# Kernel tuning notes

Hardware: AMD Instinct MI355X
Metric: run time of the kernel (lower is better)

Reference implementation:

```python
import jax, jax.numpy as jnp
import numpy as np

H, DK, DV = 16, 128, 128
EPS = 1e-6


def _causal_dw_conv(x, w):
    # depthwise causal conv, no bias. x: [B,T,C], w: [K,C]
    K = w.shape[0]
    T = x.shape[1]
    xp = jnp.pad(x, ((0, 0), (K - 1, 0), (0, 0)))
    out = w[0] * xp[:, 0:T, :]
    for i in range(1, K):
        out = out + w[i] * xp[:, i:i + T, :]
    return out


def _rmsnorm(h, w):
    hf = h.astype(jnp.float32)
    var = jnp.mean(hf * hf, axis=-1, keepdims=True)
    return (hf * jax.lax.rsqrt(var + EPS)).astype(h.dtype) * w


def _l2norm(x):
    return x * jax.lax.rsqrt(jnp.sum(x * x, axis=-1, keepdims=True) + EPS)


def setup_inputs() -> dict:
    key = jax.random.key(0)
    ks = jax.random.split(key, 32)
    B, T, D = 1, 1024, 2048
    LOW, I = 128, 8192
    KD, VD = H * DK, H * DV
    s = 0.02
    f = jnp.float32
    return {
        "x": jax.random.normal(ks[0], (B, T, D), f),
        "wq": jax.random.normal(ks[1], (D, KD), f) * s,
        "wk": jax.random.normal(ks[2], (D, KD), f) * s,
        "wv": jax.random.normal(ks[3], (D, VD), f) * s,
        "conv_q": jax.random.normal(ks[4], (4, KD), f) * 0.2,
        "conv_k": jax.random.normal(ks[5], (4, KD), f) * 0.2,
        "conv_v": jax.random.normal(ks[6], (4, VD), f) * 0.2,
        "wfa": jax.random.normal(ks[7], (D, LOW), f) * s,
        "wfb": jax.random.normal(ks[8], (LOW, H), f) * s,
        "wb": jax.random.normal(ks[9], (D, H), f) * s,
        "wga": jax.random.normal(ks[10], (D, LOW), f) * s,
        "wgb": jax.random.normal(ks[11], (LOW, VD), f) * s,
        "a_log": jax.random.normal(ks[12], (H,), f) * 0.1,
        "dt_bias": jnp.ones((H,), f),
        "o_norm_w": jnp.ones((DV,), f),
        "wo": jax.random.normal(ks[13], (VD, D), f) * s,
        "ln1_w": jnp.ones((D,), f),
        "ln2_w": jnp.ones((D,), f),
        "w_gate": jax.random.normal(ks[14], (D, I), f) * s,
        "w_up": jax.random.normal(ks[15], (D, I), f) * s,
        "w_down": jax.random.normal(ks[16], (I, D), f) * s,
    }


def reference(x, wq, wk, wv, conv_q, conv_k, conv_v, wfa, wfb, wb, wga, wgb,
              a_log, dt_bias, o_norm_w, wo, ln1_w, ln2_w, w_gate, w_up, w_down):
    B, T, D = x.shape
    # ---- pre-attention RMSNorm ----
    h = _rmsnorm(x, ln1_w)
    # ---- KDA: projections + causal depthwise conv + silu ----
    q = jax.nn.silu(_causal_dw_conv(h @ wq, conv_q)).reshape(B, T, H, DK)
    k = jax.nn.silu(_causal_dw_conv(h @ wk, conv_k)).reshape(B, T, H, DK)
    v = jax.nn.silu(_causal_dw_conv(h @ wv, conv_v)).reshape(B, T, H, DV)
    q = _l2norm(q) * (DK ** -0.5)
    k = _l2norm(k)
    # decay gate (per head, log-space, negative) and beta update gate
    g = -jnp.exp(a_log) * jax.nn.softplus((h @ wfa) @ wfb + dt_bias)  # [B,T,H]
    beta = jax.nn.sigmoid(h @ wb)                                      # [B,T,H]

    # ---- gated delta-rule linear attention (recurrent scan over time) ----
    def step(S, inp):
        qt, kt, vt, gt, bt = inp                 # [B,H,Dk],[B,H,Dk],[B,H,Dv],[B,H],[B,H]
        S = S * jnp.exp(gt)[..., None, None]     # decay state [B,H,Dk,Dv]
        kS = jnp.einsum('bhk,bhkv->bhv', kt, S)  # current prediction for k_t
        S = S + bt[..., None, None] * (kt[..., :, None] * (vt - kS)[..., None, :])
        ot = jnp.einsum('bhk,bhkv->bhv', qt, S)
        return S, ot

    S0 = jnp.zeros((B, H, DK, DV), x.dtype)
    xs = (q.transpose(1, 0, 2, 3), k.transpose(1, 0, 2, 3), v.transpose(1, 0, 2, 3),
          g.transpose(1, 0, 2), beta.transpose(1, 0, 2))
    _, o = jax.lax.scan(step, S0, xs)
    o = o.transpose(1, 0, 2, 3)                  # [B,T,H,Dv]

    # ---- gated RMSNorm on output + output projection ----
    gate = ((h @ wga) @ wgb).reshape(B, T, H, DV)
    o = _rmsnorm(o, o_norm_w) * jax.nn.silu(gate.astype(jnp.float32))
    o = o.astype(x.dtype).reshape(B, T, H * DV) @ wo
    x = x + o
    # ---- MLP block (SwiGLU) ----
    h2 = _rmsnorm(x, ln2_w)
    mlp = (jax.nn.silu(h2 @ w_gate) * (h2 @ w_up)) @ w_down
    return x + mlp
```

## Files before the change

### kernel.cpp

```cpp
#include <hip/hip_runtime.h>
#include <hip/hip_bf16.h>

typedef __attribute__((ext_vector_type(8))) short short8;
typedef __attribute__((ext_vector_type(4))) float f32x4;
typedef __attribute__((ext_vector_type(8))) unsigned short u16x8;
typedef __attribute__((ext_vector_type(4))) unsigned short u16x4;

__device__ __forceinline__ unsigned short f2bf(float f) {
  unsigned u = __float_as_uint(f);
  u += 0x7fffu + ((u >> 16) & 1u);
  return (unsigned short)(u >> 16);
}
__device__ __forceinline__ float silu_f(float x) { return x / (1.f + __expf(-x)); }
__device__ __forceinline__ float red16(float v) {
  v += __shfl_xor(v, 1); v += __shfl_xor(v, 2);
  v += __shfl_xor(v, 4); v += __shfl_xor(v, 8);
  return v;
}
template <int CTRL>
__device__ __forceinline__ float dpp_mv(float v) {
  return __int_as_float(__builtin_amdgcn_update_dpp(0, __float_as_int(v), CTRL, 0xF, 0xF, true));
}
__device__ __forceinline__ float red16d(float v) {
  v += dpp_mv<0xB1>(v);
  v += dpp_mv<0x4E>(v);
  v += dpp_mv<0x141>(v);
  v += dpp_mv<0x140>(v);
  return v;
}
__device__ __forceinline__ void gload16(const void* g, void* l) {
  __builtin_amdgcn_global_load_lds((const __attribute__((address_space(1))) void*)g,
                                   (__attribute__((address_space(3))) void*)l, 16, 0, 0);
}

struct TDesc { const float* src; unsigned short* dst; int R, C, tilesX, start; };
struct TDescs { TDesc d[11]; };

__global__ void __launch_bounds__(256) trans_all_kernel(TDescs ds) {
  __shared__ float tile[64][65];
  const int bid = blockIdx.x;
  int e = 0;
#pragma unroll
  for (int i = 1; i < 11; i++) e = (bid >= ds.d[i].start) ? i : e;
  const float* __restrict__ src = ds.d[e].src;
  unsigned short* __restrict__ dst = ds.d[e].dst;
  const int R = ds.d[e].R, C = ds.d[e].C;
  const int local = bid - ds.d[e].start;
  const int c0 = (local % ds.d[e].tilesX) * 64;
  const int r0 = (local / ds.d[e].tilesX) * 64;
  const int tid = threadIdx.x;
  const int l = tid & 15, g = tid >> 4;
#pragma unroll
  for (int i = 0; i < 4; i++) {
    const int r = r0 + g + 16 * i;
    const int c = c0 + 4 * l;
    if (r < R) {
      if (c + 3 < C) {
        float4 v = *(const float4*)(src + (size_t)r * C + c);
        tile[4 * l + 0][g + 16 * i] = v.x;
        tile[4 * l + 1][g + 16 * i] = v.y;
        tile[4 * l + 2][g + 16 * i] = v.z;
        tile[4 * l + 3][g + 16 * i] = v.w;
      } else {
#pragma unroll
        for (int j = 0; j < 4; j++)
          if (c + j < C) tile[4 * l + j][g + 16 * i] = src[(size_t)r * C + c + j];
      }
    }
  }
  __syncthreads();
#pragma unroll
  for (int i = 0; i < 4; i++) {
    const int cc = c0 + g + 16 * i;
    const int rc = r0 + 4 * l;
    if (cc < C) {
      if (rc + 3 < R) {
        u16x4 o;
        o[0] = f2bf(tile[g + 16 * i][4 * l + 0]);
        o[1] = f2bf(tile[g + 16 * i][4 * l + 1]);
        o[2] = f2bf(tile[g + 16 * i][4 * l + 2]);
        o[3] = f2bf(tile[g + 16 * i][4 * l + 3]);
        *(u16x4*)(dst + (size_t)cc * R + rc) = o;
      } else {
#pragma unroll
        for (int j = 0; j < 4; j++)
          if (rc + j < R) dst[(size_t)cc * R + rc + j] = f2bf(tile[g + 16 * i][4 * l + j]);
      }
    }
  }
}

__global__ void __launch_bounds__(256) rmsnorm_bf16_kernel(const float* __restrict__ x,
                                                           const float* __restrict__ w,
                                                           unsigned short* __restrict__ outb) {
  const int t = blockIdx.x, tid = threadIdx.x;
  const float* xr = x + (size_t)t * 2048 + tid * 8;
  float4 v0 = *(const float4*)xr, v1 = *(const float4*)(xr + 4);
  float ss = v0.x*v0.x + v0.y*v0.y + v0.z*v0.z + v0.w*v0.w
           + v1.x*v1.x + v1.y*v1.y + v1.z*v1.z + v1.w*v1.w;
#pragma unroll
  for (int m = 1; m < 64; m <<= 1) ss += __shfl_xor(ss, m);
  __shared__ float sb[4];
  if ((tid & 63) == 0) sb[tid >> 6] = ss;
  __syncthreads();
  float rn = rsqrtf((sb[0] + sb[1] + sb[2] + sb[3]) * (1.f / 2048.f) + 1e-6f);
  const float* wr = w + tid * 8;
  float4 w0 = *(const float4*)wr, w1 = *(const float4*)(wr + 4);
  u16x8 r;
  r[0]=f2bf(v0.x*rn*w0.x); r[1]=f2bf(v0.y*rn*w0.y); r[2]=f2bf(v0.z*rn*w0.z); r[3]=f2bf(v0.w*rn*w0.w);
  r[4]=f2bf(v1.x*rn*w1.x); r[5]=f2bf(v1.y*rn*w1.y); r[6]=f2bf(v1.z*rn*w1.z); r[7]=f2bf(v1.w*rn*w1.w);
  *(u16x8*)(outb + (size_t)t * 2048 + tid * 8) = r;
}

__global__ void __launch_bounds__(256) add5_rmsnorm_kernel(const float* __restrict__ x,
                                                           const float* __restrict__ y1,
                                                           const float* __restrict__ y2,
                                                           const float* __restrict__ y3,
                                                           const float* __restrict__ y4,
                                                           const float* __restrict__ w,
                                                           float* __restrict__ x1,
                                                           unsigned short* __restrict__ h2b) {
  const int t = blockIdx.x, tid = threadIdx.x;
  const int c = tid * 8;
  const size_t off = (size_t)t * 2048 + c;
  float s[8]; float ss = 0.f;
  float4 a0 = *(const float4*)(x + off),  a1 = *(const float4*)(x + off + 4);
  float4 b0 = *(const float4*)(y1 + off), b1 = *(const float4*)(y1 + off + 4);
  float4 c0 = *(const float4*)(y2 + off), c1 = *(const float4*)(y2 + off + 4);
  float4 d0 = *(const float4*)(y3 + off), d1 = *(const float4*)(y3 + off + 4);
  float4 e0 = *(const float4*)(y4 + off), e1 = *(const float4*)(y4 + off + 4);
  s[0]=a0.x+b0.x+c0.x+d0.x+e0.x; s[1]=a0.y+b0.y+c0.y+d0.y+e0.y;
  s[2]=a0.z+b0.z+c0.z+d0.z+e0.z; s[3]=a0.w+b0.w+c0.w+d0.w+e0.w;
  s[4]=a1.x+b1.x+c1.x+d1.x+e1.x; s[5]=a1.y+b1.y+c1.y+d1.y+e1.y;
  s[6]=a1.z+b1.z+c1.z+d1.z+e1.z; s[7]=a1.w+b1.w+c1.w+d1.w+e1.w;
#pragma unroll
  for (int j = 0; j < 8; j++) ss += s[j] * s[j];
#pragma unroll
  for (int m = 1; m < 64; m <<= 1) ss += __shfl_xor(ss, m);
  __shared__ float sb[4];
  if ((tid & 63) == 0) sb[tid >> 6] = ss;
  __syncthreads();
  float rn = rsqrtf((sb[0] + sb[1] + sb[2] + sb[3]) * (1.f / 2048.f) + 1e-6f);
  float* xo = x1 + off;
  *(float4*)xo = *(float4*)&s[0];
  *(float4*)(xo + 4) = *(float4*)&s[4];
  const float* wr = w + c;
  float4 w0 = *(const float4*)wr, w1 = *(const float4*)(wr + 4);
  float wv[8] = {w0.x,w0.y,w0.z,w0.w,w1.x,w1.y,w1.z,w1.w};
  u16x8 r;
#pragma unroll
  for (int j = 0; j < 8; j++) r[j] = f2bf(s[j] * rn * wv[j]);
  *(u16x8*)(h2b + off) = r;
}

__global__ void __launch_bounds__(256) gemm_bt_kernel(const unsigned short* __restrict__ A,
                                                      const unsigned short* __restrict__ Bt,
                                                      float* __restrict__ C,
                                                      int M, int N, int K, int lda, int ldb) {
  __shared__ unsigned short As[128][32];
  __shared__ unsigned short Bs[128][32];
  const int tid = threadIdx.x;
  const int m0 = blockIdx.x << 7, n0 = blockIdx.y << 7;
  const int wave = tid >> 6, lane = tid & 63;
  const int wm = (wave >> 1) << 6, wn = (wave & 1) << 6;
  const int lrow = lane >> 2, lcol = lane & 3;
  const int ar0 = wave * 16 + lrow;
  const int ar1 = ar0 + 64;
  int br0 = n0 + ar0; br0 = br0 < N ? br0 : N - 1;
  int br1 = n0 + ar1; br1 = br1 < N ? br1 : N - 1;
  const unsigned short* Aptr0 = A + (size_t)(m0 + ar0) * lda + ((lcol ^ (ar0 & 3)) << 3);
  const unsigned short* Aptr1 = A + (size_t)(m0 + ar1) * lda + ((lcol ^ (ar1 & 3)) << 3);
  const unsigned short* Bptr0 = Bt + (size_t)br0 * ldb + ((lcol ^ (ar0 & 3)) << 3);
  const unsigned short* Bptr1 = Bt + (size_t)br1 * ldb + ((lcol ^ (ar1 & 3)) << 3);
  unsigned short* lA0 = &As[wave * 16][0];
  unsigned short* lA1 = &As[64 + wave * 16][0];
  unsigned short* lB0 = &Bs[wave * 16][0];
  unsigned short* lB1 = &Bs[64 + wave * 16][0];
  const int frow = lane & 15, fkb = lane >> 4;
  f32x4 acc[4][4];
#pragma unroll
  for (int i = 0; i < 4; i++)
#pragma unroll
    for (int j = 0; j < 4; j++) acc[i][j] = (f32x4){0.f, 0.f, 0.f, 0.f};

  for (int k0 = 0; k0 < K; k0 += 32) {
    gload16(Aptr0 + k0, lA0);
    gload16(Aptr1 + k0, lA1);
    gload16(Bptr0 + k0, lB0);
    gload16(Bptr1 + k0, lB1);
    __syncthreads();
    short8 af[4], bfr[4];
#pragma unroll
    for (int i = 0; i < 4; i++) {
      int ra = wm + i * 16 + frow;
      af[i] = *(const short8*)&As[ra][(fkb ^ (ra & 3)) << 3];
      int rb = wn + i * 16 + frow;
      bfr[i] = *(const short8*)&Bs[rb][(fkb ^ (rb & 3)) << 3];
    }
#pragma unroll
    for (int i = 0; i < 4; i++)
#pragma unroll
      for (int j = 0; j < 4; j++)
        acc[i][j] = __builtin_amdgcn_mfma_f32_16x16x32_bf16(af[i], bfr[j], acc[i][j], 0, 0, 0);
    __syncthreads();
  }
  const int crow = (lane >> 4) << 2, ccol = lane & 15;
#pragma unroll
  for (int i = 0; i < 4; i++) {
    const int gr = m0 + wm + i * 16 + crow;
#pragma unroll
    for (int j = 0; j < 4; j++) {
      const int gc = n0 + wn + j * 16 + ccol;
      if (gc < N) {
#pragma unroll
        for (int r = 0; r < 4; r++) C[(size_t)(gr + r) * N + gc] = acc[i][j][r];
      }
    }
  }
}

__global__ void __launch_bounds__(256) gemm_bt_splitk4_kernel(const unsigned short* __restrict__ Abase,
                                                              const unsigned short* __restrict__ Btbase,
                                                              float* __restrict__ C0,
                                                              float* __restrict__ C1,
                                                              float* __restrict__ C2,
                                                              float* __restrict__ C3,
                                                              int M, int N, int Kq,
                                                              int lda, int ldb) {
  const unsigned short* A = Abase + (size_t)blockIdx.z * Kq;
  const unsigned short* Bt = Btbase + (size_t)blockIdx.z * Kq;
  float* C = (blockIdx.z == 0) ? C0 : (blockIdx.z == 1) ? C1 : (blockIdx.z == 2) ? C2 : C3;
  __shared__ unsigned short As[128][32];
  __shared__ unsigned short Bs[128][32];
  const int tid = threadIdx.x;
  const int m0 = blockIdx.x << 7, n0 = blockIdx.y << 7;
  const int wave = tid >> 6, lane = tid & 63;
  const int wm = (wave >> 1) << 6, wn = (wave & 1) << 6;
  const int lrow = lane >> 2, lcol = lane & 3;
  const int ar0 = wave * 16 + lrow;
  const int ar1 = ar0 + 64;
  int br0 = n0 + ar0; br0 = br0 < N ? br0 : N - 1;
  int br1 = n0 + ar1; br1 = br1 < N ? br1 : N - 1;
  const unsigned short* Aptr0 = A + (size_t)(m0 + ar0) * lda + ((lcol ^ (ar0 & 3)) << 3);
  const unsigned short* Aptr1 = A + (size_t)(m0 + ar1) * lda + ((lcol ^ (ar1 & 3)) << 3);
  const unsigned short* Bptr0 = Bt + (size_t)br0 * ldb + ((lcol ^ (ar0 & 3)) << 3);
  const unsigned short* Bptr1 = Bt + (size_t)br1 * ldb + ((lcol ^ (ar1 & 3)) << 3);
  unsigned short* lA0 = &As[wave * 16][0];
  unsigned short* lA1 = &As[64 + wave * 16][0];
  unsigned short* lB0 = &Bs[wave * 16][0];
  unsigned short* lB1 = &Bs[64 + wave * 16][0];
  const int frow = lane & 15, fkb = lane >> 4;
  f32x4 acc[4][4];
#pragma unroll
  for (int i = 0; i < 4; i++)
#pragma unroll
    for (int j = 0; j < 4; j++) acc[i][j] = (f32x4){0.f, 0.f, 0.f, 0.f};

  for (int k0 = 0; k0 < Kq; k0 += 32) {
    gload16(Aptr0 + k0, lA0);
    gload16(Aptr1 + k0, lA1);
    gload16(Bptr0 + k0, lB0);
    gload16(Bptr1 + k0, lB1);
    __syncthreads();
    short8 af[4], bfr[4];
#pragma unroll
    for (int i = 0; i < 4; i++) {
      int ra = wm + i * 16 + frow;
      af[i] = *(const short8*)&As[ra][(fkb ^ (ra & 3)) << 3];
      int rb = wn + i * 16 + frow;
      bfr[i] = *(const short8*)&Bs[rb][(fkb ^ (rb & 3)) << 3];
    }
#pragma unroll
    for (int i = 0; i < 4; i++)
#pragma unroll
      for (int j = 0; j < 4; j++)
        acc[i][j] = __builtin_amdgcn_mfma_f32_16x16x32_bf16(af[i], bfr[j], acc[i][j], 0, 0, 0);
    __syncthreads();
  }
  const int crow = (lane >> 4) << 2, ccol = lane & 15;
#pragma unroll
  for (int i = 0; i < 4; i++) {
    const int gr = m0 + wm + i * 16 + crow;
#pragma unroll
    for (int j = 0; j < 4; j++) {
      const int gc = n0 + wn + j * 16 + ccol;
      if (gc < N) {
#pragma unroll
        for (int r = 0; r < 4; r++) C[(size_t)(gr + r) * N + gc] = acc[i][j][r];
      }
    }
  }
}

__global__ void __launch_bounds__(256) gemm_dual_swiglu_kernel(const unsigned short* __restrict__ A,
                                                               const unsigned short* __restrict__ Bt,
                                                               unsigned short* __restrict__ mid) {
  __shared__ unsigned short As[128][32];
  __shared__ unsigned short B1s[128][32];
  __shared__ unsigned short B2s[128][32];
  const int tid = threadIdx.x;
  const int m0 = blockIdx.x << 7, n0 = blockIdx.y << 7;
  const int wave = tid >> 6, lane = tid & 63;
  const int wm = (wave >> 1) << 6, wn = (wave & 1) << 6;
  const int lrow = lane >> 2, lcol = lane & 3;
  const int ar0 = wave * 16 + lrow;
  const int ar1 = ar0 + 64;
  const unsigned short* Aptr0 = A + (size_t)(m0 + ar0) * 2048 + ((lcol ^ (ar0 & 3)) << 3);
  const unsigned short* Aptr1 = A + (size_t)(m0 + ar1) * 2048 + ((lcol ^ (ar1 & 3)) << 3);
  const unsigned short* B1p0 = Bt + (size_t)(n0 + ar0) * 2048 + ((lcol ^ (ar0 & 3)) << 3);
  const unsigned short* B1p1 = Bt + (size_t)(n0 + ar1) * 2048 + ((lcol ^ (ar1 & 3)) << 3);
  const unsigned short* B2p0 = B1p0 + (size_t)8192 * 2048;
  const unsigned short* B2p1 = B1p1 + (size_t)8192 * 2048;
  unsigned short* lA0 = &As[wave * 16][0];
  unsigned short* lA1 = &As[64 + wave * 16][0];
  unsigned short* lB10 = &B1s[wave * 16][0];
  unsigned short* lB11 = &B1s[64 + wave * 16][0];
  unsigned short* lB20 = &B2s[wave * 16][0];
  unsigned short* lB21 = &B2s[64 + wave * 16][0];
  const int frow = lane & 15, fkb = lane >> 4;
  f32x4 acc1[4][4], acc2[4][4];
#pragma unroll
  for (int i = 0; i < 4; i++)
#pragma unroll
    for (int j = 0; j < 4; j++) {
      acc1[i][j] = (f32x4){0.f, 0.f, 0.f, 0.f};
      acc2[i][j] = (f32x4){0.f, 0.f, 0.f, 0.f};
    }
  for (int k0 = 0; k0 < 2048; k0 += 32) {
    gload16(Aptr0 + k0, lA0);
    gload16(Aptr1 + k0, lA1);
    gload16(B1p0 + k0, lB10);
    gload16(B1p1 + k0, lB11);
    gload16(B2p0 + k0, lB20);
    gload16(B2p1 + k0, lB21);
    __syncthreads();
    short8 af[4], b1f[4], b2f[4];
#pragma unroll
    for (int i = 0; i < 4; i++) {
      int ra = wm + i * 16 + frow;
      af[i] = *(const short8*)&As[ra][(fkb ^ (ra & 3)) << 3];
      int rb = wn + i * 16 + frow;
      b1f[i] = *(const short8*)&B1s[rb][(fkb ^ (rb & 3)) << 3];
      b2f[i] = *(const short8*)&B2s[rb][(fkb ^ (rb & 3)) << 3];
    }
#pragma unroll
    for (int i = 0; i < 4; i++)
#pragma unroll
      for (int j = 0; j < 4; j++) {
        acc1[i][j] = __builtin_amdgcn_mfma_f32_16x16x32_bf16(af[i], b1f[j], acc1[i][j], 0, 0, 0);
        acc2[i][j] = __builtin_amdgcn_mfma_f32_16x16x32_bf16(af[i], b2f[j], acc2[i][j], 0, 0, 0);
      }
    __syncthreads();
  }
  const int crow = (lane >> 4) << 2, ccol = lane & 15;
#pragma unroll
  for (int i = 0; i < 4; i++) {
    const int gr = m0 + wm + i * 16 + crow;
#pragma unroll
    for (int j = 0; j < 4; j++) {
      const int gc = n0 + wn + j * 16 + ccol;
#pragma unroll
      for (int r = 0; r < 4; r++)
        mid[(size_t)(gr + r) * 8192 + gc] = f2bf(silu_f(acc1[i][j][r]) * acc2[i][j][r]);
    }
  }
}

__global__ void __launch_bounds__(256) conv_gates_kernel(const float* __restrict__ proj,
                                                         const float* __restrict__ cq,
                                                         const float* __restrict__ ck,
                                                         const float* __restrict__ cv,
                                                         const float* __restrict__ small,
                                                         const float* __restrict__ wfb,
                                                         const float* __restrict__ a_log,
                                                         const float* __restrict__ dtb,
                                                         float* __restrict__ q, float* __restrict__ k,
                                                         float* __restrict__ v,
                                                         float4* __restrict__ g4,
                                                         unsigned short* __restrict__ gab) {
  __shared__ float qksh[16];
  const int t = blockIdx.x, tid = threadIdx.x;
  const int c = tid << 3;
  float aq[8] = {0,0,0,0,0,0,0,0}, ak[8] = {0,0,0,0,0,0,0,0}, av[8] = {0,0,0,0,0,0,0,0};
#pragma unroll
  for (int i = 0; i < 4; i++) {
    const int tt = t + i - 3;
    if (tt < 0) continue;
    const float* pr = proj + (size_t)tt * 6144;
    float pq[8], pk[8], pv[8], w0[8], w1[8], w2[8];
    *(float4*)&pq[0] = *(const float4*)(pr + c);        *(float4*)&pq[4] = *(const float4*)(pr + c + 4);
    *(float4*)&pk[0] = *(const float4*)(pr + 2048 + c); *(float4*)&pk[4] = *(const float4*)(pr + 2048 + c + 4);
    *(float4*)&pv[0] = *(const float4*)(pr + 4096 + c); *(float4*)&pv[4] = *(const float4*)(pr + 4096 + c + 4);
    *(float4*)&w0[0] = *(const float4*)(cq + i * 2048 + c); *(float4*)&w0[4] = *(const float4*)(cq + i * 2048 + c + 4);
    *(float4*)&w1[0] = *(const float4*)(ck + i * 2048 + c); *(float4*)&w1[4] = *(const float4*)(ck + i * 2048 + c + 4);
    *(float4*)&w2[0] = *(const float4*)(cv + i * 2048 + c); *(float4*)&w2[4] = *(const float4*)(cv + i * 2048 + c + 4);
#pragma unroll
    for (int j = 0; j < 8; j++) { aq[j] += w0[j]*pq[j]; ak[j] += w1[j]*pk[j]; av[j] += w2[j]*pv[j]; }
  }
  float sq[8], sk[8], sv[8]; float ssq = 0.f, ssk = 0.f;
#pragma unroll
  for (int j = 0; j < 8; j++) {
    sq[j] = silu_f(aq[j]); ssq += sq[j]*sq[j];
    sk[j] = silu_f(ak[j]); ssk += sk[j]*sk[j];
    sv[j] = silu_f(av[j]);
  }
  ssq = red16(ssq); ssk = red16(ssk);
  const float rq = rsqrtf(ssq + 1e-6f) * 0.08838834764831845f;
  const float rk = rsqrtf(ssk + 1e-6f);
  float oq[8], ok[8]; float qkl = 0.f;
#pragma unroll
  for (int j = 0; j < 8; j++) { oq[j] = sq[j]*rq; ok[j] = sk[j]*rk; qkl += oq[j]*ok[j]; }
  qkl = red16(qkl);
  if ((tid & 15) == 0) qksh[tid >> 4] = qkl;
  float* qo = q + (size_t)t * 2048 + c;
  *(float4*)qo = *(float4*)&oq[0]; *(float4*)(qo + 4) = *(float4*)&oq[4];
  float* ko = k + (size_t)t * 2048 + c;
  *(float4*)ko = *(float4*)&ok[0]; *(float4*)(ko + 4) = *(float4*)&ok[4];
  float* vo = v + (size_t)t * 2048 + c;
  *(float4*)vo = *(float4*)&sv[0]; *(float4*)(vo + 4) = *(float4*)&sv[4];
  __syncthreads();
  if (tid < 128) {
    const float* srow = small + (size_t)t * 272;
    const int hh = tid >> 3, j = tid & 7;
    float d = 0.f;
#pragma unroll
    for (int i = 0; i < 16; i++) d += srow[j * 16 + i] * wfb[(j * 16 + i) * 16 + hh];
    d += __shfl_xor(d, 1); d += __shfl_xor(d, 2); d += __shfl_xor(d, 4);
    if (j == 0) {
      d += dtb[hh];
      float sp = (d > 20.f) ? d : log1pf(expf(d));
      float eg = expf(-expf(a_log[hh]) * sp);
      float bt = 1.f / (1.f + expf(-srow[128 + hh]));
      g4[t * 16 + hh] = make_float4(eg, bt, qksh[hh], 0.f);
    }
    gab[(size_t)t * 128 + tid] = f2bf(srow[144 + tid]);
  }
}

struct Slot { float4 k0, k1, q0, q1; float eg, qk, btv, bteg; };

__device__ __forceinline__ void load_slot(Slot& X, const float* kb, const float* qb,
                                          const float* vb, const float4* g4b, int tt) {
  const float* kp = kb + (size_t)tt * 2048;
  const float* qp = qb + (size_t)tt * 2048;
  X.k0 = *(const float4*)kp; X.k1 = *(const float4*)(kp + 4);
  X.q0 = *(const float4*)qp; X.q1 = *(const float4*)(qp + 4);
  float4 g = g4b[(size_t)tt * 16];
  float v = vb[(size_t)tt * 2048];
  X.eg = g.x; X.qk = g.z;
  X.btv = g.y * v;
  X.bteg = g.y * g.x;
}

__device__ __forceinline__ void step_slot(const Slot& X, float (&S)[8], float* ob,
                                          bool dostore, int tt) {
  float a0 = fmaf(X.k1.x, S[4], X.k0.x * S[0]);
  float a1 = fmaf(X.k1.y, S[5], X.k0.y * S[1]);
  float a2 = fmaf(X.k1.z, S[6], X.k0.z * S[2]);
  float a3 = fmaf(X.k1.w, S[7], X.k0.w * S[3]);
  float b0 = fmaf(X.q1.x, S[4], X.q0.x * S[0]);
  float b1 = fmaf(X.q1.y, S[5], X.q0.y * S[1]);
  float b2 = fmaf(X.q1.z, S[6], X.q0.z * S[2]);
  float b3 = fmaf(X.q1.w, S[7], X.q0.w * S[3]);
  float kS = red16d((a0 + a1) + (a2 + a3));
  float qS = red16d((b0 + b1) + (b2 + b3));
  float delta = fmaf(-X.bteg, kS, X.btv);
  S[0] = fmaf(X.k0.x, delta, X.eg * S[0]);
  S[1] = fmaf(X.k0.y, delta, X.eg * S[1]);
  S[2] = fmaf(X.k0.z, delta, X.eg * S[2]);
  S[3] = fmaf(X.k0.w, delta, X.eg * S[3]);
  S[4] = fmaf(X.k1.x, delta, X.eg * S[4]);
  S[5] = fmaf(X.k1.y, delta, X.eg * S[5]);
  S[6] = fmaf(X.k1.z, delta, X.eg * S[6]);
  S[7] = fmaf(X.k1.w, delta, X.eg * S[7]);
  if (dostore) ob[(size_t)tt * 2048] = fmaf(X.qk, delta, X.eg * qS);
}

__global__ void __launch_bounds__(64, 1) scan_kernel(const float* __restrict__ q,
                                                     const float* __restrict__ k,
                                                     const float* __restrict__ v,
                                                     const float4* __restrict__ g4,
                                                     float* __restrict__ o) {
  const int b = blockIdx.x;
  const int xcd = b & 7, r = b >> 3;
  const int h = (xcd << 1) | (r >> 5);
  const int vbase = (r & 31) << 2;
  const int lane = threadIdx.x;
  const int kl = lane & 15, vl = lane >> 4;
  const int vcol = vbase + vl;
  const int koff = h * 128 + kl * 8;
  const int voff = h * 128 + vcol;
  const float* kb = k + koff;
  const float* qb = q + koff;
  const float* vb = v + voff;
  const float4* g4b = g4 + h;
  float* ob = o + voff;
  const bool dostore = (kl == 0);
  float S[8] = {0,0,0,0,0,0,0,0};
  Slot s0, s1, s2, s3, s4, s5, s6, s7;
  load_slot(s0, kb, qb, vb, g4b, 0);
  load_slot(s1, kb, qb, vb, g4b, 1);
  load_slot(s2, kb, qb, vb, g4b, 2);
  load_slot(s3, kb, qb, vb, g4b, 3);
  load_slot(s4, kb, qb, vb, g4b, 4);
  load_slot(s5, kb, qb, vb, g4b, 5);
  load_slot(s6, kb, qb, vb, g4b, 6);
  load_slot(s7, kb, qb, vb, g4b, 7);
  for (int t = 0; t < 1024; t += 8) {
    step_slot(s0, S, ob, dostore, t + 0); load_slot(s0, kb, qb, vb, g4b, t + 8);
    step_slot(s1, S, ob, dostore, t + 1); load_slot(s1, kb, qb, vb, g4b, t + 9);
    step_slot(s2, S, ob, dostore, t + 2); load_slot(s2, kb, qb, vb, g4b, t + 10);
    step_slot(s3, S, ob, dostore, t + 3); load_slot(s3, kb, qb, vb, g4b, t + 11);
    step_slot(s4, S, ob, dostore, t + 4); load_slot(s4, kb, qb, vb, g4b, t + 12);
    step_slot(s5, S, ob, dostore, t + 5); load_slot(s5, kb, qb, vb, g4b, t + 13);
    step_slot(s6, S, ob, dostore, t + 6); load_slot(s6, kb, qb, vb, g4b, t + 14);
    step_slot(s7, S, ob, dostore, t + 7); load_slot(s7, kb, qb, vb, g4b, t + 15);
  }
}

__global__ void __launch_bounds__(256) gate_o_kernel(const float* __restrict__ o,
                                                     const float* __restrict__ gate,
                                                     const float* __restrict__ onw,
                                                     unsigned short* __restrict__ ogb) {
  const int t = blockIdx.x, tid = threadIdx.x;
  const int c = tid << 3;
  const float* orow = o + (size_t)t * 2048 + c;
  float ov[8]; *(float4*)&ov[0] = *(const float4*)orow; *(float4*)&ov[4] = *(const float4*)(orow + 4);
  float ss = 0.f;
#pragma unroll
  for (int j = 0; j < 8; j++) ss += ov[j] * ov[j];
  ss = red16(ss);
  const float rn = rsqrtf(ss * (1.f / 128.f) + 1e-6f);
  const int dv = (tid & 15) << 3;
  float wv[8]; *(float4*)&wv[0] = *(const float4*)(onw + dv); *(float4*)&wv[4] = *(const float4*)(onw + dv + 4);
  const float* grow = gate + (size_t)t * 2048 + c;
  float gv[8]; *(float4*)&gv[0] = *(const float4*)grow; *(float4*)&gv[4] = *(const float4*)(grow + 4);
  u16x8 r;
#pragma unroll
  for (int j = 0; j < 8; j++) r[j] = f2bf(ov[j] * rn * wv[j] * silu_f(gv[j]));
  *(u16x8*)(ogb + (size_t)t * 2048 + c) = r;
}

__global__ void final_add5_kernel(const float* __restrict__ a, const float* __restrict__ p0,
                                  const float* __restrict__ p1, const float* __restrict__ p2,
                                  const float* __restrict__ p3, float* __restrict__ out) {
  const int NU = 1024 * 512;
  for (int u = blockIdx.x * blockDim.x + threadIdx.x; u < NU; u += gridDim.x * blockDim.x) {
    float4 va = ((const float4*)a)[u];
    float4 v0 = ((const float4*)p0)[u];
    float4 v1 = ((const float4*)p1)[u];
    float4 v2 = ((const float4*)p2)[u];
    float4 v3 = ((const float4*)p3)[u];
    va.x += v0.x + v1.x + v2.x + v3.x;
    va.y += v0.y + v1.y + v2.y + v3.y;
    va.z += v0.z + v1.z + v2.z + v3.z;
    va.w += v0.w + v1.w + v2.w + v3.w;
    ((float4*)out)[u] = va;
  }
}

constexpr size_t SZ_WQKVT   = (size_t)6144 * 2048 * 2;
constexpr size_t SZ_WSMALLT = (size_t)272 * 2048 * 2;
constexpr size_t SZ_WGBT    = (size_t)2048 * 128 * 2;
constexpr size_t SZ_WOT     = (size_t)2048 * 2048 * 2;
constexpr size_t SZ_WMLP1T  = (size_t)16384 * 2048 * 2;
constexpr size_t SZ_WDOWNT  = (size_t)2048 * 8192 * 2;
constexpr size_t OFF_WQKVT   = 0;
constexpr size_t OFF_WSMALLT = OFF_WQKVT + SZ_WQKVT;
constexpr size_t OFF_WGBT    = OFF_WSMALLT + SZ_WSMALLT;
constexpr size_t OFF_WOT     = OFF_WGBT + SZ_WGBT;
constexpr size_t OFF_WMLP1T  = OFF_WOT + SZ_WOT;
constexpr size_t OFF_WDOWNT  = OFF_WMLP1T + SZ_WMLP1T;
constexpr size_t A0          = OFF_WDOWNT + SZ_WDOWNT;
constexpr size_t OFF_HB    = A0;
constexpr size_t OFF_PROJ  = OFF_HB + (size_t)1024 * 2048 * 2;
constexpr size_t OFF_SMALL = OFF_PROJ + (size_t)1024 * 6144 * 4;
constexpr size_t OFF_Q     = OFF_SMALL + (size_t)1024 * 272 * 4;
constexpr size_t OFF_K     = OFF_Q + (size_t)1024 * 2048 * 4;
constexpr size_t OFF_V     = OFF_K + (size_t)1024 * 2048 * 4;
constexpr size_t OFF_G     = OFF_V + (size_t)1024 * 2048 * 4;
constexpr size_t OFF_BETA  = OFF_G + (size_t)1024 * 16 * 4;
constexpr size_t OFF_GAB   = OFF_BETA + (size_t)1024 * 16 * 4;
constexpr size_t OFF_GATE  = OFF_GAB + (size_t)1024 * 128 * 2;
constexpr size_t OFF_O     = OFF_GATE + (size_t)1024 * 2048 * 4;
constexpr size_t OFF_OGB   = OFF_O + (size_t)1024 * 2048 * 4;
constexpr size_t OFF_OPROJ = OFF_OGB + (size_t)1024 * 2048 * 2;
constexpr size_t OFF_X1    = OFF_OPROJ + (size_t)1024 * 2048 * 4;
constexpr size_t OFF_H2B   = OFF_X1 + (size_t)1024 * 2048 * 4;
constexpr size_t OFF_MID    = A0 + (size_t)1024 * 16384 * 4;
constexpr size_t OFF_MLPOUT = OFF_H2B + (size_t)1024 * 2048 * 2;
constexpr size_t OFF_QKB    = OFF_MLPOUT + (size_t)1024 * 2048 * 4;
constexpr size_t OFF_G4     = OFF_QKB + (size_t)1024 * 16 * 4;
constexpr size_t OFF_MLPOUT2= OFF_G4 + (size_t)1040 * 16 * 16;
constexpr size_t WS_NEED    = OFF_MLPOUT2 + (size_t)1024 * 2048 * 4;
constexpr size_t OFF_OPROJ2 = OFF_O;
constexpr size_t OFF_OPROJ3 = OFF_PROJ;
constexpr size_t OFF_OPROJ4 = OFF_PROJ + (size_t)1024 * 2048 * 4;
constexpr size_t OFF_MLPOUT3 = OFF_Q;
constexpr size_t OFF_MLPOUT4 = OFF_K;

extern "C" void kernel_launch(void* const* d_in, const int* in_sizes, int n_in,
                              void* d_out, int out_size, void* d_ws, size_t ws_size,
                              hipStream_t stream) {
  (void)in_sizes; (void)n_in; (void)out_size;
  const float* x     = (const float*)d_in[0];
  const float* wq    = (const float*)d_in[1];
  const float* wk    = (const float*)d_in[2];
  const float* wv    = (const float*)d_in[3];
  const float* cq    = (const float*)d_in[4];
  const float* ck    = (const float*)d_in[5];
  const float* cv    = (const float*)d_in[6];
  const float* wfa   = (const float*)d_in[7];
  const float* wfb   = (const float*)d_in[8];
  const float* wb    = (const float*)d_in[9];
  const float* wga   = (const float*)d_in[10];
  const float* wgb   = (const float*)d_in[11];
  const float* a_log = (const float*)d_in[12];
  const float* dtb   = (const float*)d_in[13];
  const float* onw   = (const float*)d_in[14];
  const float* wo    = (const float*)d_in[15];
  const float* ln1   = (const float*)d_in[16];
  const float* ln2   = (const float*)d_in[17];
  const float* wgate = (const float*)d_in[18];
  const float* wup   = (const float*)d_in[19];
  const float* wdown = (const float*)d_in[20];
  float* out = (float*)d_out;
  char* ws = (char*)d_ws;
  if (ws_size < WS_NEED) return;

  unsigned short* wqkvT   = (unsigned short*)(ws + OFF_WQKVT);
  unsigned short* wsmallT = (unsigned short*)(ws + OFF_WSMALLT);
  unsigned short* wgbT    = (unsigned short*)(ws + OFF_WGBT);
  unsigned short* woT     = (unsigned short*)(ws + OFF_WOT);
  unsigned short* wmlp1T  = (unsigned short*)(ws + OFF_WMLP1T);
  unsigned short* wdownT  = (unsigned short*)(ws + OFF_WDOWNT);
  unsigned short* hb      = (unsigned short*)(ws + OFF_HB);
  float* projf  = (float*)(ws + OFF_PROJ);
  float* smallf = (float*)(ws + OFF_SMALL);
  float* qf     = (float*)(ws + OFF_Q);
  float* kf     = (float*)(ws + OFF_K);
  float* vf     = (float*)(ws + OFF_V);
  unsigned short* gab = (unsigned short*)(ws + OFF_GAB);
  float* gatef  = (float*)(ws + OFF_GATE);
  float* of     = (float*)(ws + OFF_O);
  unsigned short* ogb = (unsigned short*)(ws + OFF_OGB);
  float* oprojf = (float*)(ws + OFF_OPROJ);
  float* oproj2f= (float*)(ws + OFF_OPROJ2);
  float* oproj3f= (float*)(ws + OFF_OPROJ3);
  float* oproj4f= (float*)(ws + OFF_OPROJ4);
  float* x1f    = (float*)(ws + OFF_X1);
  unsigned short* h2b = (unsigned short*)(ws + OFF_H2B);
  unsigned short* midb = (unsigned short*)(ws + OFF_MID);
  float* mlpoutf  = (float*)(ws + OFF_MLPOUT);
  float* mlpout2f = (float*)(ws + OFF_MLPOUT2);
  float* mlpout3f = (float*)(ws + OFF_MLPOUT3);
  float* mlpout4f = (float*)(ws + OFF_MLPOUT4);
  float4* g4    = (float4*)(ws + OFF_G4);

  TDescs tds;
  int st = 0;
  auto set = [&](int i, const float* s, unsigned short* d, int R, int C) {
    int tx = (C + 63) / 64, ty = (R + 63) / 64;
    tds.d[i] = TDesc{s, d, R, C, tx, st};
    st += tx * ty;
  };
  set(0, wq, wqkvT, 2048, 2048);
  set(1, wk, wqkvT + (size_t)2048 * 2048, 2048, 2048);
  set(2, wv, wqkvT + (size_t)4096 * 2048, 2048, 2048);
  set(3, wfa, wsmallT, 2048, 128);
  set(4, wb, wsmallT + (size_t)128 * 2048, 2048, 16);
  set(5, wga, wsmallT + (size_t)144 * 2048, 2048, 128);
  set(6, wgb, wgbT, 128, 2048);
  set(7, wo, woT, 2048, 2048);
  set(8, wgate, wmlp1T, 2048, 8192);
  set(9, wup, wmlp1T + (size_t)8192 * 2048, 2048, 8192);
  set(10, wdown, wdownT, 8192, 2048);
  trans_all_kernel<<<st, 256, 0, stream>>>(tds);

  rmsnorm_bf16_kernel<<<1024, 256, 0, stream>>>(x, ln1, hb);
  gemm_bt_kernel<<<dim3(8, 48), 256, 0, stream>>>(hb, wqkvT, projf, 1024, 6144, 2048, 2048, 2048);
  gemm_bt_kernel<<<dim3(8, 3), 256, 0, stream>>>(hb, wsmallT, smallf, 1024, 272, 2048, 2048, 2048);
  conv_gates_kernel<<<1024, 256, 0, stream>>>(projf, cq, ck, cv, smallf, wfb, a_log, dtb,
                                              qf, kf, vf, g4, gab);
  gemm_bt_kernel<<<dim3(8, 16), 256, 0, stream>>>(gab, wgbT, gatef, 1024, 2048, 128, 128, 128);
  scan_kernel<<<512, 64, 0, stream>>>(qf, kf, vf, g4, of);
  gate_o_kernel<<<1024, 256, 0, stream>>>(of, gatef, onw, ogb);
  gemm_bt_splitk4_kernel<<<dim3(8, 16, 4), 256, 0, stream>>>(ogb, woT,
      oprojf, oproj2f, oproj3f, oproj4f, 1024, 2048, 512, 2048, 2048);
  add5_rmsnorm_kernel<<<1024, 256, 0, stream>>>(x, oprojf, oproj2f, oproj3f, oproj4f,
                                                ln2, x1f, h2b);
  gemm_dual_swiglu_kernel<<<dim3(8, 64), 256, 0, stream>>>(h2b, wmlp1T, midb);
  gemm_bt_splitk4_kernel<<<dim3(8, 16, 4), 256, 0, stream>>>(midb, wdownT,
      mlpoutf, mlpout2f, mlpout3f, mlpout4f, 1024, 2048, 2048, 8192, 8192);
  final_add5_kernel<<<2048, 256, 0, stream>>>(x1f, mlpoutf, mlpout2f, mlpout3f, mlpout4f, out);
}
```

Before: 699.0 us.

## Overlap late weight transposes with the scan and merge QKV/small GEMM launches

Transposing the wo, MLP gate/up and down weights is moved out of the upfront transpose kernel and into extra blocks of the scan kernel. The scan uses only 512 single-wave blocks, so idle CUs can do the bf16 weight conversion alongside it. The QKV projection and the small projection GEMMs are also merged into one launch via a shared gemm_body device function. The risk is that the extra transpose blocks compete with the latency-bound scan for memory bandwidth, or get scheduled ahead of scan blocks and delay them.

```diff
diff --git a/kernel.cpp b/kernel.cpp
--- a/kernel.cpp
+++ b/kernel.cpp
@@ -34,14 +34,14 @@
 }
 
 struct TDesc { const float* src; unsigned short* dst; int R, C, tilesX, start; };
-struct TDescs { TDesc d[11]; };
-
-__global__ void __launch_bounds__(256) trans_all_kernel(TDescs ds) {
+struct TDescs { TDesc d[7]; };
+
+__global__ void __launch_bounds__(256) trans_early_kernel(TDescs ds) {
   __shared__ float tile[64][65];
   const int bid = blockIdx.x;
   int e = 0;
 #pragma unroll
-  for (int i = 1; i < 11; i++) e = (bid >= ds.d[i].start) ? i : e;
+  for (int i = 1; i < 7; i++) e = (bid >= ds.d[i].start) ? i : e;
   const float* __restrict__ src = ds.d[e].src;
   unsigned short* __restrict__ dst = ds.d[e].dst;
   const int R = ds.d[e].R, C = ds.d[e].C;
@@ -153,14 +153,14 @@
   *(u16x8*)(h2b + off) = r;
 }
 
-__global__ void __launch_bounds__(256) gemm_bt_kernel(const unsigned short* __restrict__ A,
-                                                      const unsigned short* __restrict__ Bt,
-                                                      float* __restrict__ C,
-                                                      int M, int N, int K, int lda, int ldb) {
+__device__ __forceinline__ void gemm_body(const unsigned short* __restrict__ A,
+                                          const unsigned short* __restrict__ Bt,
+                                          float* __restrict__ C,
+                                          int N, int K, int lda, int ldb,
+                                          int m0, int n0) {
   __shared__ unsigned short As[128][32];
   __shared__ unsigned short Bs[128][32];
   const int tid = threadIdx.x;
-  const int m0 = blockIdx.x << 7, n0 = blockIdx.y << 7;
   const int wave = tid >> 6, lane = tid & 63;
   const int wm = (wave >> 1) << 6, wn = (wave & 1) << 6;
   const int lrow = lane >> 2, lcol = lane & 3;
@@ -219,6 +219,23 @@
   }
 }
 
+__global__ void __launch_bounds__(256) gemm_bt_kernel(const unsigned short* __restrict__ A,
+                                                      const unsigned short* __restrict__ Bt,
+                                                      float* __restrict__ C,
+                                                      int M, int N, int K, int lda, int ldb) {
+  gemm_body(A, Bt, C, N, K, lda, ldb, blockIdx.x << 7, blockIdx.y << 7);
+}
+
+__global__ void __launch_bounds__(256) gemm_qkv_small_kernel(const unsigned short* __restrict__ A,
+                                                             const unsigned short* __restrict__ Bqkv,
+                                                             const unsigned short* __restrict__ Bsmall,
+                                                             float* __restrict__ Cqkv,
+                                                             float* __restrict__ Csmall) {
+  const int by = blockIdx.y;
+  if (by < 48) gemm_body(A, Bqkv, Cqkv, 6144, 2048, 2048, 2048, blockIdx.x << 7, by << 7);
+  else         gemm_body(A, Bsmall, Csmall, 272, 2048, 2048, 2048, blockIdx.x << 7, (by - 48) << 7);
+}
+
 __global__ void __launch_bounds__(256) gemm_bt_splitk4_kernel(const unsigned short* __restrict__ Abase,
                                                               const unsigned short* __restrict__ Btbase,
                                                               float* __restrict__ C0,
@@ -230,66 +247,7 @@
   const unsigned short* A = Abase + (size_t)blockIdx.z * Kq;
   const unsigned short* Bt = Btbase + (size_t)blockIdx.z * Kq;
   float* C = (blockIdx.z == 0) ? C0 : (blockIdx.z == 1) ? C1 : (blockIdx.z == 2) ? C2 : C3;
-  __shared__ unsigned short As[128][32];
-  __shared__ unsigned short Bs[128][32];
-  const int tid = threadIdx.x;
-  const int m0 = blockIdx.x << 7, n0 = blockIdx.y << 7;
-  const int wave = tid >> 6, lane = tid & 63;
-  const int wm = (wave >> 1) << 6, wn = (wave & 1) << 6;
-  const int lrow = lane >> 2, lcol = lane & 3;
-  const int ar0 = wave * 16 + lrow;
-  const int ar1 = ar0 + 64;
-  int br0 = n0 + ar0; br0 = br0 < N ? br0 : N - 1;
-  int br1 = n0 + ar1; br1 = br1 < N ? br1 : N - 1;
-  const unsigned short* Aptr0 = A + (size_t)(m0 + ar0) * lda + ((lcol ^ (ar0 & 3)) << 3);
-  const unsigned short* Aptr1 = A + (size_t)(m0 + ar1) * lda + ((lcol ^ (ar1 & 3)) << 3);
-  const unsigned short* Bptr0 = Bt + (size_t)br0 * ldb + ((lcol ^ (ar0 & 3)) << 3);
-  const unsigned short* Bptr1 = Bt + (size_t)br1 * ldb + ((lcol ^ (ar1 & 3)) << 3);
-  unsigned short* lA0 = &As[wave * 16][0];
-  unsigned short* lA1 = &As[64 + wave * 16][0];
-  unsigned short* lB0 = &Bs[wave * 16][0];
-  unsigned short* lB1 = &Bs[64 + wave * 16][0];
-  const int frow = lane & 15, fkb = lane >> 4;
-  f32x4 acc[4][4];
-#pragma unroll
-  for (int i = 0; i < 4; i++)
-#pragma unroll
-    for (int j = 0; j < 4; j++) acc[i][j] = (f32x4){0.f, 0.f, 0.f, 0.f};
-
-  for (int k0 = 0; k0 < Kq; k0 += 32) {
-    gload16(Aptr0 + k0, lA0);
-    gload16(Aptr1 + k0, lA1);
-    gload16(Bptr0 + k0, lB0);
-    gload16(Bptr1 + k0, lB1);
-    __syncthreads();
-    short8 af[4], bfr[4];
-#pragma unroll
-    for (int i = 0; i < 4; i++) {
-      int ra = wm + i * 16 + frow;
-      af[i] = *(const short8*)&As[ra][(fkb ^ (ra & 3)) << 3];
-      int rb = wn + i * 16 + frow;
-      bfr[i] = *(const short8*)&Bs[rb][(fkb ^ (rb & 3)) << 3];
-    }
-#pragma unroll
-    for (int i = 0; i < 4; i++)
-#pragma unroll
-      for (int j = 0; j < 4; j++)
-        acc[i][j] = __builtin_amdgcn_mfma_f32_16x16x32_bf16(af[i], bfr[j], acc[i][j], 0, 0, 0);
-    __syncthreads();
-  }
-  const int crow = (lane >> 4) << 2, ccol = lane & 15;
-#pragma unroll
-  for (int i = 0; i < 4; i++) {
-    const int gr = m0 + wm + i * 16 + crow;
-#pragma unroll
-    for (int j = 0; j < 4; j++) {
-      const int gc = n0 + wn + j * 16 + ccol;
-      if (gc < N) {
-#pragma unroll
-        for (int r = 0; r < 4; r++) C[(size_t)(gr + r) * N + gc] = acc[i][j][r];
-      }
-    }
-  }
+  gemm_body(A, Bt, C, N, Kq, lda, ldb, blockIdx.x << 7, blockIdx.y << 7);
 }
 
 __global__ void __launch_bounds__(256) gemm_dual_swiglu_kernel(const unsigned short* __restrict__ A,
@@ -476,45 +434,87 @@
   if (dostore) ob[(size_t)tt * 2048] = fmaf(X.qk, delta, X.eg * qS);
 }
 
-__global__ void __launch_bounds__(64, 1) scan_kernel(const float* __restrict__ q,
-                                                     const float* __restrict__ k,
-                                                     const float* __restrict__ v,
-                                                     const float4* __restrict__ g4,
-                                                     float* __restrict__ o) {
-  const int b = blockIdx.x;
-  const int xcd = b & 7, r = b >> 3;
-  const int h = (xcd << 1) | (r >> 5);
-  const int vbase = (r & 31) << 2;
-  const int lane = threadIdx.x;
-  const int kl = lane & 15, vl = lane >> 4;
-  const int vcol = vbase + vl;
-  const int koff = h * 128 + kl * 8;
-  const int voff = h * 128 + vcol;
-  const float* kb = k + koff;
-  const float* qb = q + koff;
-  const float* vb = v + voff;
-  const float4* g4b = g4 + h;
-  float* ob = o + voff;
-  const bool dostore = (kl == 0);
-  float S[8] = {0,0,0,0,0,0,0,0};
-  Slot s0, s1, s2, s3, s4, s5, s6, s7;
-  load_slot(s0, kb, qb, vb, g4b, 0);
-  load_slot(s1, kb, qb, vb, g4b, 1);
-  load_slot(s2, kb, qb, vb, g4b, 2);
-  load_slot(s3, kb, qb, vb, g4b, 3);
-  load_slot(s4, kb, qb, vb, g4b, 4);
-  load_slot(s5, kb, qb, vb, g4b, 5);
-  load_slot(s6, kb, qb, vb, g4b, 6);
-  load_slot(s7, kb, qb, vb, g4b, 7);
-  for (int t = 0; t < 1024; t += 8) {
-    step_slot(s0, S, ob, dostore, t + 0); load_slot(s0, kb, qb, vb, g4b, t + 8);
-    step_slot(s1, S, ob, dostore, t + 1); load_slot(s1, kb, qb, vb, g4b, t + 9);
-    step_slot(s2, S, ob, dostore, t + 2); load_slot(s2, kb, qb, vb, g4b, t + 10);
-    step_slot(s3, S, ob, dostore, t + 3); load_slot(s3, kb, qb, vb, g4b, t + 11);
-    step_slot(s4, S, ob, dostore, t + 4); load_slot(s4, kb, qb, vb, g4b, t + 12);
-    step_slot(s5, S, ob, dostore, t + 5); load_slot(s5, kb, qb, vb, g4b, t + 13);
-    step_slot(s6, S, ob, dostore, t + 6); load_slot(s6, kb, qb, vb, g4b, t + 14);
-    step_slot(s7, S, ob, dostore, t + 7); load_slot(s7, kb, qb, vb, g4b, t + 15);
+struct TD4 { const float* src; unsigned short* dst; int R, C, tilesX, start; };
+struct TD4s { TD4 d[4]; int total; };
+
+__global__ void __launch_bounds__(64, 1) scan_trans_kernel(const float* __restrict__ q,
+                                                           const float* __restrict__ k,
+                                                           const float* __restrict__ v,
+                                                           const float4* __restrict__ g4,
+                                                           float* __restrict__ o,
+                                                           TD4s ds) {
+  __shared__ float tile[64][65];
+  if (blockIdx.x < 512) {
+    const int b = blockIdx.x;
+    const int xcd = b & 7, r = b >> 3;
+    const int h = (xcd << 1) | (r >> 5);
+    const int vbase = (r & 31) << 2;
+    const int lane = threadIdx.x;
+    const int kl = lane & 15, vl = lane >> 4;
+    const int vcol = vbase + vl;
+    const int koff = h * 128 + kl * 8;
+    const int voff = h * 128 + vcol;
+    const float* kb = k + koff;
+    const float* qb = q + koff;
+    const float* vb = v + voff;
+    const float4* g4b = g4 + h;
+    float* ob = o + voff;
+    const bool dostore = (kl == 0);
+    float S[8] = {0,0,0,0,0,0,0,0};
+    Slot s0, s1, s2, s3, s4, s5, s6, s7;
+    load_slot(s0, kb, qb, vb, g4b, 0);
+    load_slot(s1, kb, qb, vb, g4b, 1);
+    load_slot(s2, kb, qb, vb, g4b, 2);
+    load_slot(s3, kb, qb, vb, g4b, 3);
+    load_slot(s4, kb, qb, vb, g4b, 4);
+    load_slot(s5, kb, qb, vb, g4b, 5);
+    load_slot(s6, kb, qb, vb, g4b, 6);
+    load_slot(s7, kb, qb, vb, g4b, 7);
+    for (int t = 0; t < 1024; t += 8) {
+      step_slot(s0, S, ob, dostore, t + 0); load_slot(s0, kb, qb, vb, g4b, t + 8);
+      step_slot(s1, S, ob, dostore, t + 1); load_slot(s1, kb, qb, vb, g4b, t + 9);
+      step_slot(s2, S, ob, dostore, t + 2); load_slot(s2, kb, qb, vb, g4b, t + 10);
+      step_slot(s3, S, ob, dostore, t + 3); load_slot(s3, kb, qb, vb, g4b, t + 11);
+      step_slot(s4, S, ob, dostore, t + 4); load_slot(s4, kb, qb, vb, g4b, t + 12);
+      step_slot(s5, S, ob, dostore, t + 5); load_slot(s5, kb, qb, vb, g4b, t + 13);
+      step_slot(s6, S, ob, dostore, t + 6); load_slot(s6, kb, qb, vb, g4b, t + 14);
+      step_slot(s7, S, ob, dostore, t + 7); load_slot(s7, kb, qb, vb, g4b, t + 15);
+    }
+  } else {
+    const int tid = threadIdx.x;
+    const int l = tid & 15, g2 = tid >> 4;
+    for (int tb = blockIdx.x - 512; tb < ds.total; tb += gridDim.x - 512) {
+      int e = 0;
+#pragma unroll
+      for (int i = 1; i < 4; i++) e = (tb >= ds.d[i].start) ? i : e;
+      const float* __restrict__ src = ds.d[e].src;
+      unsigned short* __restrict__ dst = ds.d[e].dst;
+      const int R = ds.d[e].R, C = ds.d[e].C;
+      const int local = tb - ds.d[e].start;
+      const int c0 = (local % ds.d[e].tilesX) * 64;
+      const int r0 = (local / ds.d[e].tilesX) * 64;
+#pragma unroll
+      for (int ii = 0; ii < 16; ii++) {
+        const int rr = g2 + 4 * ii;
+        float4 vv = *(const float4*)(src + (size_t)(r0 + rr) * C + c0 + 4 * l);
+        tile[4 * l + 0][rr] = vv.x;
+        tile[4 * l + 1][rr] = vv.y;
+        tile[4 * l + 2][rr] = vv.z;
+        tile[4 * l + 3][rr] = vv.w;
+      }
+      __syncthreads();
+#pragma unroll
+      for (int ii = 0; ii < 16; ii++) {
+        const int cc = g2 + 4 * ii;
+        u16x4 oo;
+        oo[0] = f2bf(tile[cc][4 * l + 0]);
+        oo[1] = f2bf(tile[cc][4 * l + 1]);
+        oo[2] = f2bf(tile[cc][4 * l + 2]);
+        oo[3] = f2bf(tile[cc][4 * l + 3]);
+        *(u16x4*)(dst + (size_t)(c0 + cc) * R + r0 + 4 * l) = oo;
+      }
+      __syncthreads();
+    }
   }
 }
 
@@ -671,19 +671,27 @@
   set(4, wb, wsmallT + (size_t)128 * 2048, 2048, 16);
   set(5, wga, wsmallT + (size_t)144 * 2048, 2048, 128);
   set(6, wgb, wgbT, 128, 2048);
-  set(7, wo, woT, 2048, 2048);
-  set(8, wgate, wmlp1T, 2048, 8192);
-  set(9, wup, wmlp1T + (size_t)8192 * 2048, 2048, 8192);
-  set(10, wdown, wdownT, 8192, 2048);
-  trans_all_kernel<<<st, 256, 0, stream>>>(tds);
+  trans_early_kernel<<<st, 256, 0, stream>>>(tds);
+
+  TD4s lds4;
+  int lt = 0;
+  auto set4 = [&](int i, const float* s, unsigned short* d, int R, int C) {
+    int tx = C / 64, ty = R / 64;
+    lds4.d[i] = TD4{s, d, R, C, tx, lt};
+    lt += tx * ty;
+  };
+  set4(0, wo, woT, 2048, 2048);
+  set4(1, wgate, wmlp1T, 2048, 8192);
+  set4(2, wup, wmlp1T + (size_t)8192 * 2048, 2048, 8192);
+  set4(3, wdown, wdownT, 8192, 2048);
+  lds4.total = lt;
 
   rmsnorm_bf16_kernel<<<1024, 256, 0, stream>>>(x, ln1, hb);
-  gemm_bt_kernel<<<dim3(8, 48), 256, 0, stream>>>(hb, wqkvT, projf, 1024, 6144, 2048, 2048, 2048);
-  gemm_bt_kernel<<<dim3(8, 3), 256, 0, stream>>>(hb, wsmallT, smallf, 1024, 272, 2048, 2048, 2048);
+  gemm_qkv_small_kernel<<<dim3(8, 51), 256, 0, stream>>>(hb, wqkvT, wsmallT, projf, smallf);
   conv_gates_kernel<<<1024, 256, 0, stream>>>(projf, cq, ck, cv, smallf, wfb, a_log, dtb,
                                               qf, kf, vf, g4, gab);
   gemm_bt_kernel<<<dim3(8, 16), 256, 0, stream>>>(gab, wgbT, gatef, 1024, 2048, 128, 128, 128);
-  scan_kernel<<<512, 64, 0, stream>>>(qf, kf, vf, g4, of);
+  scan_trans_kernel<<<512 + 2048, 64, 0, stream>>>(qf, kf, vf, g4, of, lds4);
   gate_o_kernel<<<1024, 256, 0, stream>>>(of, gatef, onw, ogb);
   gemm_bt_splitk4_kernel<<<dim3(8, 16, 4), 256, 0, stream>>>(ogb, woT,
       oprojf, oproj2f, oproj3f, oproj4f, 1024, 2048, 512, 2048, 2048);
```

After: 623.7 us. -10.8%, faster.
